# Kernel tuning notes

Measured on AMD Instinct MI355X. Metric: run time of the kernel, lower is better.

The kernel has to match this reference:

```python
import jax, jax.numpy as jnp
import numpy as np

N_CORES = 64
N_QUBITS = 1024
QEMB = 256
N_EDGES = 448
BATCH = 512
NN_DIMS = (256, 512, 512, 256)


def setup_inputs() -> dict:
    key = jax.random.key(0)
    ks = jax.random.split(key, 12)
    inp = {
        "core_allocs": jax.random.randint(ks[0], (BATCH, N_QUBITS), 0, N_CORES, dtype=jnp.int32),
        "qubit_embs": jax.random.normal(ks[1], (N_QUBITS, QEMB), dtype=jnp.float32),
        "dummy_qubit_emb": jax.random.normal(ks[2], (QEMB,), dtype=jnp.float32),
        "edge_index": jax.random.randint(ks[3], (2, N_EDGES), 0, N_CORES, dtype=jnp.int32),
        "edge_weight": jax.random.uniform(ks[4], (N_EDGES,), dtype=jnp.float32),
        "W1": jax.random.normal(ks[5], (NN_DIMS[0], NN_DIMS[1]), dtype=jnp.float32) * 0.05,
        "b1": jax.random.normal(ks[6], (NN_DIMS[1],), dtype=jnp.float32) * 0.05,
        "W2": jax.random.normal(ks[7], (NN_DIMS[1], NN_DIMS[2]), dtype=jnp.float32) * 0.05,
        "b2": jax.random.normal(ks[8], (NN_DIMS[2],), dtype=jnp.float32) * 0.05,
        "W3": jax.random.normal(ks[9], (NN_DIMS[2], NN_DIMS[3]), dtype=jnp.float32) * 0.05,
        "b3": jax.random.normal(ks[10], (NN_DIMS[3],), dtype=jnp.float32) * 0.05,
    }
    return inp


def _gcn_norm(edge_index, edge_weight):
    # PyG gcn_norm: add self loops (weight 1), symmetric D^{-1/2} A D^{-1/2}.
    self_idx = jnp.arange(N_CORES, dtype=edge_index.dtype)
    row = jnp.concatenate([edge_index[0], self_idx])
    col = jnp.concatenate([edge_index[1], self_idx])
    w = jnp.concatenate([edge_weight, jnp.ones((N_CORES,), edge_weight.dtype)])
    deg = jax.ops.segment_sum(w, col, num_segments=N_CORES)  # degree at targets
    dinv = jnp.where(deg > 0, deg ** -0.5, 0.0)
    norm = dinv[row] * w * dinv[col]
    return row, col, norm


def reference(core_allocs, qubit_embs, dummy_qubit_emb, edge_index, edge_weight,
              W1, b1, W2, b2, W3, b3):
    # ---- unmixedCoreEmbs, vectorized: per-core max over assigned qubit embs,
    # dummy emb always included (cores never at capacity) ----
    def pool(alloc):  # alloc: [n_qubits] -> [n_cores, qemb]
        seg = jax.ops.segment_max(qubit_embs, alloc, num_segments=N_CORES)
        return jnp.maximum(seg, dummy_qubit_emb)  # also fixes -inf empty cores

    x = jax.vmap(pool)(core_allocs)  # [B, n_cores, qemb]

    # ---- GCNConv stack (same graph replicated per batch element) ----
    row, col, norm = _gcn_norm(edge_index, edge_weight)

    def gcn_layer(h, W, b):
        hw = h @ W  # [B, C, d_out]
        msg = hw[:, row, :] * norm[None, :, None]  # gather sources, scale
        agg = jnp.zeros((h.shape[0], N_CORES, W.shape[1]), hw.dtype).at[:, col, :].add(msg)
        return jax.nn.relu(agg + b)

    x = gcn_layer(x, W1, b1)
    x = gcn_layer(x, W2, b2)
    x = gcn_layer(x, W3, b3)
    return x  # [B, n_cores, nn_dims[-1]] (original returns this split per batch element)
```

## Files before the change

kernel.cpp:

```cpp
#include <hip/hip_runtime.h>
#include <type_traits>

typedef __attribute__((ext_vector_type(8))) short short8;
typedef __attribute__((ext_vector_type(4))) short short4v;
typedef __attribute__((ext_vector_type(2))) short short2v;
typedef __attribute__((ext_vector_type(4))) float f32x4;
typedef unsigned short u16;
typedef unsigned int u32;

#define N_EDGES 448

#define WS_ADJA 0
#define WS_ADJB 4096
#define WS_W1   8192
#define WS_W2   139264
#define WS_W3   401408
#define WS_DUM  532480
#define WS_B1   (WS_DUM + 256)
#define WS_B2   (WS_DUM + 768)
#define WS_B3   (WS_DUM + 1280)
#define WS_QE   534528
#define WS_FLAG 796672

__device__ __forceinline__ float bf2f(u16 v) {
    u32 u = ((u32)v) << 16;
    return __builtin_bit_cast(float, u);
}
__device__ __forceinline__ u16 f2bf(float f) {
    u32 u = __builtin_bit_cast(u32, f);
    u32 r = u + 0x7FFFu + ((u >> 16) & 1u);
    return (u16)(r >> 16);
}
__device__ __forceinline__ u16 f2bf_fast(float f) {
    u32 u = __builtin_bit_cast(u32, f);
    return (u16)((u + 0x8000u) >> 16);
}
__device__ __forceinline__ float ldf(const void* p, int idx, u32 isf32) {
    return isf32 ? ((const float*)p)[idx] : bf2f(((const u16*)p)[idx]);
}
__device__ __forceinline__ u16 keyb(u16 b) {
    return (u16)(b ^ ((u16)(((u16)((short)b >> 15)) >> 1)));
}
__device__ __forceinline__ u32 pkmax(u32 a, u32 b) {
    short2v x = __builtin_bit_cast(short2v, a);
    short2v y = __builtin_bit_cast(short2v, b);
    short2v r = __builtin_elementwise_max(x, y);
    return __builtin_bit_cast(u32, r);
}

__global__ __launch_bounds__(512) void prep(
    const int* __restrict__ eidx, const void* __restrict__ ew,
    const void* __restrict__ qembs, const void* __restrict__ dummy,
    const void* __restrict__ W1, const void* __restrict__ b1,
    const void* __restrict__ W2, const void* __restrict__ b2,
    const void* __restrict__ W3, const void* __restrict__ b3,
    u16* __restrict__ ws) {
    const int t = threadIdx.x, bb = blockIdx.x;
    __shared__ u32 s_isf;
    if (t < 64) {
        const u16* qs = (const u16*)qembs;
        int c = 0;
#pragma unroll
        for (int j = 0; j < 4; j++) {
            u16 v = qs[(t * 4 + j) * 2];
            u32 e = (v >> 7) & 0xFF;
            c += (e >= 100 && e <= 134) ? 1 : 0;
        }
#pragma unroll
        for (int off = 32; off > 0; off >>= 1) c += __shfl_down(c, off, 64);
        if (t == 0) s_isf = (c < 128) ? 1u : 0u;
    }
    __syncthreads();
    const u32 isf32 = s_isf;

    if (t < 128) {
        const int bw = bb * 2 + (t >> 6);
        const int tl = t & 63;
        const void* src;
        int N, K32, dst, nt, kk;
        if (bw < 256)      { src = W1; N = 512; K32 = 8;  dst = WS_W1; nt = bw / 8;          kk = bw % 8; }
        else if (bw < 768) { src = W2; N = 512; K32 = 16; dst = WS_W2; nt = (bw - 256) / 16; kk = (bw - 256) % 16; }
        else               { src = W3; N = 256; K32 = 16; dst = WS_W3; nt = (bw - 768) / 16; kk = (bw - 768) % 16; }
        const int col = nt * 16 + (tl & 15);
        const int krow = kk * 32 + (tl >> 4) * 8;
        u16 v[8];
#pragma unroll
        for (int j = 0; j < 8; j++) v[j] = f2bf(ldf(src, (krow + j) * N + col, isf32));
        u16* o = ws + dst + (nt * K32 + kk) * 512 + tl * 8;
#pragma unroll
        for (int j = 0; j < 8; j++) o[j] = v[j];
    }
    if (t >= 256) {
        const int base = bb * 512 + (t - 256) * 2;
        ws[WS_QE + base]     = keyb(f2bf(ldf(qembs, base, isf32)));
        ws[WS_QE + base + 1] = keyb(f2bf(ldf(qembs, base + 1, isf32)));
    }
    if (bb == 1) {
#pragma unroll
        for (int j = 0; j < 4; j++) {
            int i = t + j * 512;
            if (i < 1792) {
                u16 o;
                if (i < 256)       o = keyb(f2bf(ldf(dummy, i, isf32)));
                else if (i < 768)  o = f2bf(ldf(b1, i - 256, isf32));
                else if (i < 1280) o = f2bf(ldf(b2, i - 768, isf32));
                else               o = f2bf(ldf(b3, i - 1280, isf32));
                ws[WS_DUM + i] = o;
            }
        }
    }
    if (bb == 0) {
        __shared__ float A[4096];
        __shared__ float deg[64];
        __shared__ float dinv[64];
        __shared__ int er[N_EDGES];
        __shared__ int ec[N_EDGES];
        __shared__ float ewf[N_EDGES];
        if (t < N_EDGES) {
            er[t] = eidx[t];
            ec[t] = eidx[N_EDGES + t];
            ewf[t] = ldf(ew, t, isf32);
        }
        if (t < 64) deg[t] = 1.0f;
        for (int i = t; i < 4096; i += 512) A[i] = 0.f;
        __syncthreads();
        if (t < N_EDGES) atomicAdd(&deg[ec[t]], ewf[t]);
        __syncthreads();
        if (t < 64) dinv[t] = 1.0f / sqrtf(deg[t]);
        __syncthreads();
        if (t < N_EDGES) atomicAdd(&A[ec[t] * 64 + er[t]], dinv[er[t]] * ewf[t] * dinv[ec[t]]);
        __syncthreads();
        if (t < 64) A[t * 64 + t] += dinv[t] * dinv[t];
        __syncthreads();
        for (int i = t; i < 4096; i += 512) {
            int chunk = i >> 9, m = (i >> 3) & 63, j = i & 7;
            ws[WS_ADJA + i] = f2bf(A[m * 64 + chunk * 8 + j]);
        }
        for (int i = t; i < 4096; i += 512) {
            int chunk = i >> 9, l = (i >> 3) & 63, j = i & 7;
            int ntc = chunk >> 1, kk = chunk & 1;
            int k = kk * 32 + (l >> 4) * 8 + j;
            int c2 = ntc * 16 + (l & 15);
            ws[WS_ADJB + i] = f2bf(A[c2 * 64 + k]);
        }
        if (t == 0) *(u32*)(ws + WS_FLAG) = isf32;
    }
}

__global__ __launch_bounds__(1024, 4) void fused(
    const int* __restrict__ allocs, const u16* __restrict__ ws,
    void* __restrict__ out) {

    __shared__ __align__(16) u16 BUF[64 * 512];

    const int t = threadIdx.x, bb = blockIdx.x;
    const int wave = t >> 6, lane = t & 63, quad = lane >> 4, nl = lane & 15;
    const u32 isf32 = *(const u32*)(ws + WS_FLAG);

    {
        int* LIST = (int*)(BUF + 16384);
        int* CNT  = LIST + 1024;
        int* SST  = CNT + 64;
        int* WOF  = SST + 64;
        if (t < 64) CNT[t] = 0;
        __syncthreads();
        const int myc = allocs[bb * 1024 + t];
        atomicAdd(&CNT[myc], 1);
        __syncthreads();
        if (t < 64) {
            int v = CNT[t], s = v;
#pragma unroll
            for (int off = 1; off < 64; off <<= 1) {
                int u = __shfl_up(s, off, 64);
                if (t >= off) s += u;
            }
            SST[t] = s - v;
            WOF[t] = s - v;
        }
        __syncthreads();
        {
            int pos = atomicAdd(&WOF[myc], 1);
            LIST[pos] = t;
        }
        __syncthreads();
        const u16* wsq = ws + WS_QE;
        const uint2 dk = *(const uint2*)(ws + WS_DUM + lane * 4);
        for (int i = 0; i < 4; i++) {
            const int c = wave * 4 + i;
            const int L = CNT[c], S = SST[c];
            u32 m0 = dk.x, m1 = dk.y;
            int j = 0;
            for (; j + 4 <= L; j += 4) {
                const int q0 = LIST[S + j],     q1 = LIST[S + j + 1];
                const int q2 = LIST[S + j + 2], q3 = LIST[S + j + 3];
                uint2 ra = *(const uint2*)(wsq + q0 * 256 + lane * 4);
                uint2 rb = *(const uint2*)(wsq + q1 * 256 + lane * 4);
                uint2 rc = *(const uint2*)(wsq + q2 * 256 + lane * 4);
                uint2 rd = *(const uint2*)(wsq + q3 * 256 + lane * 4);
                m0 = pkmax(pkmax(m0, ra.x), pkmax(rb.x, rc.x));
                m1 = pkmax(pkmax(m1, ra.y), pkmax(rb.y, rc.y));
                m0 = pkmax(m0, rd.x);
                m1 = pkmax(m1, rd.y);
            }
            for (; j < L; j++) {
                const int q = LIST[S + j];
                uint2 r = *(const uint2*)(wsq + q * 256 + lane * 4);
                m0 = pkmax(m0, r.x);
                m1 = pkmax(m1, r.y);
            }
            short4v p;
            p[0] = (short)keyb((u16)(m0 & 0xffffu));
            p[1] = (short)keyb((u16)(m0 >> 16));
            p[2] = (short)keyb((u16)(m1 & 0xffffu));
            p[3] = (short)keyb((u16)(m1 >> 16));
            *(short4v*)(BUF + (lane >> 1) * 512 + c * 8 + (lane & 1) * 4) = p;
        }
    }
    __syncthreads();

    short8 adjB[4][2];
#pragma unroll
    for (int ntc = 0; ntc < 4; ntc++)
#pragma unroll
        for (int h = 0; h < 2; h++)
            adjB[ntc][h] = *(const short8*)(ws + WS_ADJB + (ntc * 2 + h) * 512 + lane * 8);

    auto layerT = [&](auto K32c, const u16* __restrict__ W, const u16* __restrict__ bias) {
        constexpr int K32 = decltype(K32c)::value;
        const int s0 = wave * 2;
        u16* scr = BUF + (wave * 4 + 2) * 512;
        f32x4 acc[2][4];
#pragma unroll
        for (int s = 0; s < 2; s++)
#pragma unroll
            for (int rt = 0; rt < 4; rt++) acc[s][rt] = f32x4{0.f, 0.f, 0.f, 0.f};
#pragma unroll
        for (int kk = 0; kk < K32; kk++) {
            short8 a[4], bch[2];
#pragma unroll
            for (int rt = 0; rt < 4; rt++)
                a[rt] = *(const short8*)(BUF + (kk * 4 + quad) * 512 + (rt * 16 + nl) * 8);
#pragma unroll
            for (int s = 0; s < 2; s++)
                bch[s] = *(const short8*)(W + ((s0 + s) * K32 + kk) * 512 + lane * 8);
#pragma unroll
            for (int s = 0; s < 2; s++)
#pragma unroll
                for (int rt = 0; rt < 4; rt++)
                    acc[s][rt] = __builtin_amdgcn_mfma_f32_16x16x32_bf16(a[rt], bch[s], acc[s][rt], 0, 0, 0);
        }
        __syncthreads();
#pragma unroll
        for (int s = 0; s < 2; s++) {
            const int nt = s0 + s;
            f32x4 agg[4];
#pragma unroll
            for (int ntc = 0; ntc < 4; ntc++) agg[ntc] = f32x4{0.f, 0.f, 0.f, 0.f};
#pragma unroll
            for (int h = 0; h < 2; h++) {
#pragma unroll
                for (int r2 = 0; r2 < 2; r2++) {
                    f32x4 v = acc[s][2 * h + r2];
                    short4v p;
#pragma unroll
                    for (int rr = 0; rr < 4; rr++) p[rr] = (short)f2bf_fast(v[rr]);
                    *(short4v*)(scr + nl * 40 + r2 * 16 + quad * 4) = p;
                }
                short8 hwf = *(const short8*)(scr + nl * 40 + quad * 8);
#pragma unroll
                for (int ntc = 0; ntc < 4; ntc++)
                    agg[ntc] = __builtin_amdgcn_mfma_f32_16x16x32_bf16(hwf, adjB[ntc][h], agg[ntc], 0, 0, 0);
            }
            float bv[4];
#pragma unroll
            for (int rr = 0; rr < 4; rr++) bv[rr] = bf2f(bias[nt * 16 + quad * 4 + rr]);
#pragma unroll
            for (int ntc = 0; ntc < 4; ntc++) {
                short4v p;
#pragma unroll
                for (int rr = 0; rr < 4; rr++)
                    p[rr] = (short)f2bf_fast(fmaxf(agg[ntc][rr] + bv[rr], 0.f));
                *(short4v*)(BUF + (nt * 2 + (quad >> 1)) * 512 + (ntc * 16 + nl) * 8 + (quad & 1) * 4) = p;
            }
        }
        __syncthreads();
    };

    auto layer3 = [&](const u16* __restrict__ W) {
        const int nt = wave;
        f32x4 acc[4];
#pragma unroll
        for (int rt = 0; rt < 4; rt++) acc[rt] = f32x4{0.f, 0.f, 0.f, 0.f};
#pragma unroll
        for (int kk = 0; kk < 16; kk++) {
            short8 a[4];
#pragma unroll
            for (int rt = 0; rt < 4; rt++)
                a[rt] = *(const short8*)(BUF + (kk * 4 + quad) * 512 + (rt * 16 + nl) * 8);
            short8 bch = *(const short8*)(W + (nt * 16 + kk) * 512 + lane * 8);
#pragma unroll
            for (int rt = 0; rt < 4; rt++)
                acc[rt] = __builtin_amdgcn_mfma_f32_16x16x32_bf16(a[rt], bch, acc[rt], 0, 0, 0);
        }
        __syncthreads();
        u16* scr = BUF + 16384 + wave * 640;
#pragma unroll
        for (int h = 0; h < 2; h++) {
#pragma unroll
            for (int r2 = 0; r2 < 2; r2++) {
                f32x4 v = acc[2 * h + r2];
                short4v p;
#pragma unroll
                for (int rr = 0; rr < 4; rr++) p[rr] = (short)f2bf_fast(v[rr]);
                *(short4v*)(scr + nl * 40 + r2 * 16 + quad * 4) = p;
            }
            short8 hwf = *(const short8*)(scr + nl * 40 + quad * 8);
            *(short8*)(BUF + (nt * 2 + h) * 512 + lane * 8) = hwf;
        }
        __syncthreads();
    };

    layerT(std::integral_constant<int, 8>{},  ws + WS_W1, ws + WS_B1);
    layerT(std::integral_constant<int, 16>{}, ws + WS_W2, ws + WS_B2);
    layer3(ws + WS_W3);

    {
        const int rt2 = wave & 3, nt0 = (wave >> 2) * 4;
        short8 aA[2];
#pragma unroll
        for (int h = 0; h < 2; h++)
            aA[h] = *(const short8*)(ws + WS_ADJA + (h * 4 + quad) * 512 + (rt2 * 16 + nl) * 8);
        f32x4 accv[4];
#pragma unroll
        for (int ni = 0; ni < 4; ni++) {
            const int nt = nt0 + ni;
            short8 b0v = *(const short8*)(BUF + (nt * 2 + 0) * 512 + lane * 8);
            short8 b1v = *(const short8*)(BUF + (nt * 2 + 1) * 512 + lane * 8);
            f32x4 a = f32x4{0.f, 0.f, 0.f, 0.f};
            a = __builtin_amdgcn_mfma_f32_16x16x32_bf16(aA[0], b0v, a, 0, 0, 0);
            a = __builtin_amdgcn_mfma_f32_16x16x32_bf16(aA[1], b1v, a, 0, 0, 0);
            accv[ni] = a;
        }
        __syncthreads();
        float* Hf = (float*)BUF;
#pragma unroll
        for (int ni = 0; ni < 4; ni++) {
            const int n = (nt0 + ni) * 16 + nl;
            const float bv = bf2f(ws[WS_B3 + n]);
#pragma unroll
            for (int rr = 0; rr < 4; rr++) {
                const int m2 = rt2 * 16 + quad * 4 + rr;
                Hf[m2 * 256 + n] = fmaxf(accv[ni][rr] + bv, 0.f);
            }
        }
        __syncthreads();
        if (isf32) {
            float4* outv = (float4*)((float*)out + (size_t)bb * 16384);
            const float4* Hv = (const float4*)Hf;
#pragma unroll
            for (int p4 = 0; p4 < 4; p4++) outv[p4 * 1024 + t] = Hv[p4 * 1024 + t];
        } else {
            u16* outu = (u16*)out + (size_t)bb * 16384;
#pragma unroll
            for (int p4 = 0; p4 < 4; p4++) {
                const int idx = (p4 * 1024 + t) * 4;
                float4 v = *(const float4*)(Hf + idx);
                short4v pk;
                pk[0] = (short)f2bf_fast(v.x); pk[1] = (short)f2bf_fast(v.y);
                pk[2] = (short)f2bf_fast(v.z); pk[3] = (short)f2bf_fast(v.w);
                *(short4v*)(outu + idx) = pk;
            }
        }
    }
}

extern "C" void kernel_launch(void* const* d_in, const int* in_sizes, int n_in,
                              void* d_out, int out_size, void* d_ws, size_t ws_size,
                              hipStream_t stream) {
    const int* allocs = (const int*)d_in[0];
    const void* qembs = d_in[1];
    const void* dummy = d_in[2];
    const int* eidx   = (const int*)d_in[3];
    const void* ew    = d_in[4];
    const void* W1 = d_in[5];
    const void* b1 = d_in[6];
    const void* W2 = d_in[7];
    const void* b2 = d_in[8];
    const void* W3 = d_in[9];
    const void* b3 = d_in[10];
    u16* ws = (u16*)d_ws;

    prep<<<512, 512, 0, stream>>>(eidx, ew, qembs, dummy, W1, b1, W2, b2, W3, b3, ws);
    fused<<<512, 1024, 0, stream>>>(allocs, ws, d_out);
}
```

Baseline: 148.8 us.

## Process two batch elements per block to reuse weight fragments

Each block now handles two batch elements with double LDS buffers, so every weight fragment loaded from global memory feeds the MFMAs of both elements. The grid shrinks from 512 to 256 blocks. The adjacency B fragments move from registers into a shared-memory copy to save registers. The cost is double the LDS per block (about 136KB), which likely allows only one block per CU and leaves 256 blocks for a 256-CU device, so latency hiding and occupancy may suffer.

```diff
diff --git a/kernel.cpp b/kernel.cpp
--- a/kernel.cpp
+++ b/kernel.cpp
@@ -151,171 +151,204 @@
     const int* __restrict__ allocs, const u16* __restrict__ ws,
     void* __restrict__ out) {
 
-    __shared__ __align__(16) u16 BUF[64 * 512];
+    __shared__ __align__(16) u16 BUF[2][64 * 512];
+    __shared__ __align__(16) u16 ADJB_S[4096];
 
     const int t = threadIdx.x, bb = blockIdx.x;
     const int wave = t >> 6, lane = t & 63, quad = lane >> 4, nl = lane & 15;
     const u32 isf32 = *(const u32*)(ws + WS_FLAG);
+    const int e0 = bb * 2;
+
+    if (t < 512) *(uint4*)(ADJB_S + t * 8) = *(const uint4*)(ws + WS_ADJB + t * 8);
 
     {
-        int* LIST = (int*)(BUF + 16384);
-        int* CNT  = LIST + 1024;
-        int* SST  = CNT + 64;
-        int* WOF  = SST + 64;
-        if (t < 64) CNT[t] = 0;
-        __syncthreads();
-        const int myc = allocs[bb * 1024 + t];
-        atomicAdd(&CNT[myc], 1);
-        __syncthreads();
-        if (t < 64) {
-            int v = CNT[t], s = v;
+        int* LISTA = (int*)(BUF[0] + 16384);
+        int* CNTA  = LISTA + 1024;
+        int* SSTA  = CNTA + 64;
+        int* WOFA  = SSTA + 64;
+        int* LISTB = (int*)(BUF[1] + 16384);
+        int* CNTB  = LISTB + 1024;
+        int* SSTB  = CNTB + 64;
+        int* WOFB  = SSTB + 64;
+        if (t < 64) { CNTA[t] = 0; CNTB[t] = 0; }
+        __syncthreads();
+        const int ca = allocs[e0 * 1024 + t];
+        const int cb = allocs[(e0 + 1) * 1024 + t];
+        atomicAdd(&CNTA[ca], 1);
+        atomicAdd(&CNTB[cb], 1);
+        __syncthreads();
+        if (t < 128) {
+            const int l = t & 63;
+            int* C  = (t < 64) ? CNTA : CNTB;
+            int* S  = (t < 64) ? SSTA : SSTB;
+            int* Wo = (t < 64) ? WOFA : WOFB;
+            int v = C[l], s = v;
 #pragma unroll
             for (int off = 1; off < 64; off <<= 1) {
                 int u = __shfl_up(s, off, 64);
-                if (t >= off) s += u;
-            }
-            SST[t] = s - v;
-            WOF[t] = s - v;
+                if (l >= off) s += u;
+            }
+            S[l] = s - v;
+            Wo[l] = s - v;
         }
         __syncthreads();
         {
-            int pos = atomicAdd(&WOF[myc], 1);
-            LIST[pos] = t;
+            int pa = atomicAdd(&WOFA[ca], 1); LISTA[pa] = t;
+            int pb = atomicAdd(&WOFB[cb], 1); LISTB[pb] = t;
         }
         __syncthreads();
         const u16* wsq = ws + WS_QE;
         const uint2 dk = *(const uint2*)(ws + WS_DUM + lane * 4);
-        for (int i = 0; i < 4; i++) {
-            const int c = wave * 4 + i;
-            const int L = CNT[c], S = SST[c];
-            u32 m0 = dk.x, m1 = dk.y;
-            int j = 0;
-            for (; j + 4 <= L; j += 4) {
-                const int q0 = LIST[S + j],     q1 = LIST[S + j + 1];
-                const int q2 = LIST[S + j + 2], q3 = LIST[S + j + 3];
-                uint2 ra = *(const uint2*)(wsq + q0 * 256 + lane * 4);
-                uint2 rb = *(const uint2*)(wsq + q1 * 256 + lane * 4);
-                uint2 rc = *(const uint2*)(wsq + q2 * 256 + lane * 4);
-                uint2 rd = *(const uint2*)(wsq + q3 * 256 + lane * 4);
-                m0 = pkmax(pkmax(m0, ra.x), pkmax(rb.x, rc.x));
-                m1 = pkmax(pkmax(m1, ra.y), pkmax(rb.y, rc.y));
-                m0 = pkmax(m0, rd.x);
-                m1 = pkmax(m1, rd.y);
-            }
-            for (; j < L; j++) {
-                const int q = LIST[S + j];
-                uint2 r = *(const uint2*)(wsq + q * 256 + lane * 4);
-                m0 = pkmax(m0, r.x);
-                m1 = pkmax(m1, r.y);
-            }
-            short4v p;
-            p[0] = (short)keyb((u16)(m0 & 0xffffu));
-            p[1] = (short)keyb((u16)(m0 >> 16));
-            p[2] = (short)keyb((u16)(m1 & 0xffffu));
-            p[3] = (short)keyb((u16)(m1 >> 16));
-            *(short4v*)(BUF + (lane >> 1) * 512 + c * 8 + (lane & 1) * 4) = p;
+#pragma unroll
+        for (int e = 0; e < 2; e++) {
+            const int* LIST = e ? LISTB : LISTA;
+            const int* CNT  = e ? CNTB  : CNTA;
+            const int* SST  = e ? SSTB  : SSTA;
+            u16* XB = BUF[e];
+            for (int i = 0; i < 4; i++) {
+                const int c = wave * 4 + i;
+                const int L = CNT[c], S = SST[c];
+                u32 m0 = dk.x, m1 = dk.y;
+                int j = 0;
+                for (; j + 4 <= L; j += 4) {
+                    const int q0 = LIST[S + j],     q1 = LIST[S + j + 1];
+                    const int q2 = LIST[S + j + 2], q3 = LIST[S + j + 3];
+                    uint2 ra = *(const uint2*)(wsq + q0 * 256 + lane * 4);
+                    uint2 rb = *(const uint2*)(wsq + q1 * 256 + lane * 4);
+                    uint2 rc = *(const uint2*)(wsq + q2 * 256 + lane * 4);
+                    uint2 rd = *(const uint2*)(wsq + q3 * 256 + lane * 4);
+                    m0 = pkmax(pkmax(m0, ra.x), pkmax(rb.x, rc.x));
+                    m1 = pkmax(pkmax(m1, ra.y), pkmax(rb.y, rc.y));
+                    m0 = pkmax(m0, rd.x);
+                    m1 = pkmax(m1, rd.y);
+                }
+                for (; j < L; j++) {
+                    const int q = LIST[S + j];
+                    uint2 r = *(const uint2*)(wsq + q * 256 + lane * 4);
+                    m0 = pkmax(m0, r.x);
+                    m1 = pkmax(m1, r.y);
+                }
+                short4v p;
+                p[0] = (short)keyb((u16)(m0 & 0xffffu));
+                p[1] = (short)keyb((u16)(m0 >> 16));
+                p[2] = (short)keyb((u16)(m1 & 0xffffu));
+                p[3] = (short)keyb((u16)(m1 >> 16));
+                *(short4v*)(XB + (lane >> 1) * 512 + c * 8 + (lane & 1) * 4) = p;
+            }
         }
     }
     __syncthreads();
-
-    short8 adjB[4][2];
-#pragma unroll
-    for (int ntc = 0; ntc < 4; ntc++)
-#pragma unroll
-        for (int h = 0; h < 2; h++)
-            adjB[ntc][h] = *(const short8*)(ws + WS_ADJB + (ntc * 2 + h) * 512 + lane * 8);
 
     auto layerT = [&](auto K32c, const u16* __restrict__ W, const u16* __restrict__ bias) {
         constexpr int K32 = decltype(K32c)::value;
         const int s0 = wave * 2;
-        u16* scr = BUF + (wave * 4 + 2) * 512;
-        f32x4 acc[2][4];
-#pragma unroll
-        for (int s = 0; s < 2; s++)
-#pragma unroll
-            for (int rt = 0; rt < 4; rt++) acc[s][rt] = f32x4{0.f, 0.f, 0.f, 0.f};
+        f32x4 acc[2][2][4];
+#pragma unroll
+        for (int e = 0; e < 2; e++)
+#pragma unroll
+            for (int s = 0; s < 2; s++)
+#pragma unroll
+                for (int rt = 0; rt < 4; rt++) acc[e][s][rt] = f32x4{0.f, 0.f, 0.f, 0.f};
 #pragma unroll
         for (int kk = 0; kk < K32; kk++) {
-            short8 a[4], bch[2];
-#pragma unroll
-            for (int rt = 0; rt < 4; rt++)
-                a[rt] = *(const short8*)(BUF + (kk * 4 + quad) * 512 + (rt * 16 + nl) * 8);
+            short8 bch[2];
 #pragma unroll
             for (int s = 0; s < 2; s++)
                 bch[s] = *(const short8*)(W + ((s0 + s) * K32 + kk) * 512 + lane * 8);
 #pragma unroll
-            for (int s = 0; s < 2; s++)
+            for (int e = 0; e < 2; e++) {
+                short8 a[4];
 #pragma unroll
                 for (int rt = 0; rt < 4; rt++)
-                    acc[s][rt] = __builtin_amdgcn_mfma_f32_16x16x32_bf16(a[rt], bch[s], acc[s][rt], 0, 0, 0);
+                    a[rt] = *(const short8*)(BUF[e] + (kk * 4 + quad) * 512 + (rt * 16 + nl) * 8);
+#pragma unroll
+                for (int s = 0; s < 2; s++)
+#pragma unroll
+                    for (int rt = 0; rt < 4; rt++)
+                        acc[e][s][rt] = __builtin_amdgcn_mfma_f32_16x16x32_bf16(a[rt], bch[s], acc[e][s][rt], 0, 0, 0);
+            }
         }
         __syncthreads();
 #pragma unroll
         for (int s = 0; s < 2; s++) {
             const int nt = s0 + s;
-            f32x4 agg[4];
-#pragma unroll
-            for (int ntc = 0; ntc < 4; ntc++) agg[ntc] = f32x4{0.f, 0.f, 0.f, 0.f};
+            float bv[4];
+#pragma unroll
+            for (int rr = 0; rr < 4; rr++) bv[rr] = bf2f(bias[nt * 16 + quad * 4 + rr]);
+#pragma unroll
+            for (int e = 0; e < 2; e++) {
+                u16* scr = BUF[e] + (wave * 4 + 2) * 512;
+                f32x4 agg[4];
+#pragma unroll
+                for (int ntc = 0; ntc < 4; ntc++) agg[ntc] = f32x4{0.f, 0.f, 0.f, 0.f};
+#pragma unroll
+                for (int h = 0; h < 2; h++) {
+#pragma unroll
+                    for (int r2 = 0; r2 < 2; r2++) {
+                        f32x4 v = acc[e][s][2 * h + r2];
+                        short4v p;
+#pragma unroll
+                        for (int rr = 0; rr < 4; rr++) p[rr] = (short)f2bf_fast(v[rr]);
+                        *(short4v*)(scr + nl * 40 + r2 * 16 + quad * 4) = p;
+                    }
+                    short8 hwf = *(const short8*)(scr + nl * 40 + quad * 8);
+#pragma unroll
+                    for (int ntc = 0; ntc < 4; ntc++) {
+                        short8 bfrag = *(const short8*)(ADJB_S + (ntc * 2 + h) * 512 + lane * 8);
+                        agg[ntc] = __builtin_amdgcn_mfma_f32_16x16x32_bf16(hwf, bfrag, agg[ntc], 0, 0, 0);
+                    }
+                }
+#pragma unroll
+                for (int ntc = 0; ntc < 4; ntc++) {
+                    short4v p;
+#pragma unroll
+                    for (int rr = 0; rr < 4; rr++)
+                        p[rr] = (short)f2bf_fast(fmaxf(agg[ntc][rr] + bv[rr], 0.f));
+                    *(short4v*)(BUF[e] + (nt * 2 + (quad >> 1)) * 512 + (ntc * 16 + nl) * 8 + (quad & 1) * 4) = p;
+                }
+            }
+        }
+        __syncthreads();
+    };
+
+    auto layer3 = [&](const u16* __restrict__ W) {
+        const int nt = wave;
+        f32x4 acc[2][4];
+#pragma unroll
+        for (int e = 0; e < 2; e++)
+#pragma unroll
+            for (int rt = 0; rt < 4; rt++) acc[e][rt] = f32x4{0.f, 0.f, 0.f, 0.f};
+#pragma unroll
+        for (int kk = 0; kk < 16; kk++) {
+            short8 bch = *(const short8*)(W + (nt * 16 + kk) * 512 + lane * 8);
+#pragma unroll
+            for (int e = 0; e < 2; e++) {
+                short8 a[4];
+#pragma unroll
+                for (int rt = 0; rt < 4; rt++)
+                    a[rt] = *(const short8*)(BUF[e] + (kk * 4 + quad) * 512 + (rt * 16 + nl) * 8);
+#pragma unroll
+                for (int rt = 0; rt < 4; rt++)
+                    acc[e][rt] = __builtin_amdgcn_mfma_f32_16x16x32_bf16(a[rt], bch, acc[e][rt], 0, 0, 0);
+            }
+        }
+        __syncthreads();
+#pragma unroll
+        for (int e = 0; e < 2; e++) {
+            u16* scr = BUF[e] + 16384 + wave * 640;
 #pragma unroll
             for (int h = 0; h < 2; h++) {
 #pragma unroll
                 for (int r2 = 0; r2 < 2; r2++) {
-                    f32x4 v = acc[s][2 * h + r2];
+                    f32x4 v = acc[e][2 * h + r2];
                     short4v p;
 #pragma unroll
                     for (int rr = 0; rr < 4; rr++) p[rr] = (short)f2bf_fast(v[rr]);
                     *(short4v*)(scr + nl * 40 + r2 * 16 + quad * 4) = p;
                 }
                 short8 hwf = *(const short8*)(scr + nl * 40 + quad * 8);
-#pragma unroll
-                for (int ntc = 0; ntc < 4; ntc++)
-                    agg[ntc] = __builtin_amdgcn_mfma_f32_16x16x32_bf16(hwf, adjB[ntc][h], agg[ntc], 0, 0, 0);
-            }
-            float bv[4];
-#pragma unroll
-            for (int rr = 0; rr < 4; rr++) bv[rr] = bf2f(bias[nt * 16 + quad * 4 + rr]);
-#pragma unroll
-            for (int ntc = 0; ntc < 4; ntc++) {
-                short4v p;
-#pragma unroll
-                for (int rr = 0; rr < 4; rr++)
-                    p[rr] = (short)f2bf_fast(fmaxf(agg[ntc][rr] + bv[rr], 0.f));
-                *(short4v*)(BUF + (nt * 2 + (quad >> 1)) * 512 + (ntc * 16 + nl) * 8 + (quad & 1) * 4) = p;
-            }
-        }
-        __syncthreads();
-    };
-
-    auto layer3 = [&](const u16* __restrict__ W) {
-        const int nt = wave;
-        f32x4 acc[4];
-#pragma unroll
-        for (int rt = 0; rt < 4; rt++) acc[rt] = f32x4{0.f, 0.f, 0.f, 0.f};
-#pragma unroll
-        for (int kk = 0; kk < 16; kk++) {
-            short8 a[4];
-#pragma unroll
-            for (int rt = 0; rt < 4; rt++)
-                a[rt] = *(const short8*)(BUF + (kk * 4 + quad) * 512 + (rt * 16 + nl) * 8);
-            short8 bch = *(const short8*)(W + (nt * 16 + kk) * 512 + lane * 8);
-#pragma unroll
-            for (int rt = 0; rt < 4; rt++)
-                acc[rt] = __builtin_amdgcn_mfma_f32_16x16x32_bf16(a[rt], bch, acc[rt], 0, 0, 0);
-        }
-        __syncthreads();
-        u16* scr = BUF + 16384 + wave * 640;
-#pragma unroll
-        for (int h = 0; h < 2; h++) {
-#pragma unroll
-            for (int r2 = 0; r2 < 2; r2++) {
-                f32x4 v = acc[2 * h + r2];
-                short4v p;
-#pragma unroll
-                for (int rr = 0; rr < 4; rr++) p[rr] = (short)f2bf_fast(v[rr]);
-                *(short4v*)(scr + nl * 40 + r2 * 16 + quad * 4) = p;
-            }
-            short8 hwf = *(const short8*)(scr + nl * 40 + quad * 8);
-            *(short8*)(BUF + (nt * 2 + h) * 512 + lane * 8) = hwf;
+                *(short8*)(BUF[e] + (nt * 2 + h) * 512 + lane * 8) = hwf;
+            }
         }
         __syncthreads();
     };
@@ -330,45 +363,57 @@
 #pragma unroll
         for (int h = 0; h < 2; h++)
             aA[h] = *(const short8*)(ws + WS_ADJA + (h * 4 + quad) * 512 + (rt2 * 16 + nl) * 8);
-        f32x4 accv[4];
-#pragma unroll
-        for (int ni = 0; ni < 4; ni++) {
-            const int nt = nt0 + ni;
-            short8 b0v = *(const short8*)(BUF + (nt * 2 + 0) * 512 + lane * 8);
-            short8 b1v = *(const short8*)(BUF + (nt * 2 + 1) * 512 + lane * 8);
-            f32x4 a = f32x4{0.f, 0.f, 0.f, 0.f};
-            a = __builtin_amdgcn_mfma_f32_16x16x32_bf16(aA[0], b0v, a, 0, 0, 0);
-            a = __builtin_amdgcn_mfma_f32_16x16x32_bf16(aA[1], b1v, a, 0, 0, 0);
-            accv[ni] = a;
-        }
-        __syncthreads();
-        float* Hf = (float*)BUF;
-#pragma unroll
-        for (int ni = 0; ni < 4; ni++) {
-            const int n = (nt0 + ni) * 16 + nl;
-            const float bv = bf2f(ws[WS_B3 + n]);
-#pragma unroll
-            for (int rr = 0; rr < 4; rr++) {
-                const int m2 = rt2 * 16 + quad * 4 + rr;
-                Hf[m2 * 256 + n] = fmaxf(accv[ni][rr] + bv, 0.f);
+        f32x4 accv[2][4];
+#pragma unroll
+        for (int e = 0; e < 2; e++)
+#pragma unroll
+            for (int ni = 0; ni < 4; ni++) {
+                const int nt = nt0 + ni;
+                short8 b0v = *(const short8*)(BUF[e] + (nt * 2 + 0) * 512 + lane * 8);
+                short8 b1v = *(const short8*)(BUF[e] + (nt * 2 + 1) * 512 + lane * 8);
+                f32x4 a = f32x4{0.f, 0.f, 0.f, 0.f};
+                a = __builtin_amdgcn_mfma_f32_16x16x32_bf16(aA[0], b0v, a, 0, 0, 0);
+                a = __builtin_amdgcn_mfma_f32_16x16x32_bf16(aA[1], b1v, a, 0, 0, 0);
+                accv[e][ni] = a;
+            }
+        __syncthreads();
+#pragma unroll
+        for (int e = 0; e < 2; e++) {
+            float* Hf = (float*)BUF[e];
+#pragma unroll
+            for (int ni = 0; ni < 4; ni++) {
+                const int n = (nt0 + ni) * 16 + nl;
+                const float bv = bf2f(ws[WS_B3 + n]);
+#pragma unroll
+                for (int rr = 0; rr < 4; rr++) {
+                    const int m2 = rt2 * 16 + quad * 4 + rr;
+                    Hf[m2 * 256 + n] = fmaxf(accv[e][ni][rr] + bv, 0.f);
+                }
             }
         }
         __syncthreads();
         if (isf32) {
-            float4* outv = (float4*)((float*)out + (size_t)bb * 16384);
-            const float4* Hv = (const float4*)Hf;
-#pragma unroll
-            for (int p4 = 0; p4 < 4; p4++) outv[p4 * 1024 + t] = Hv[p4 * 1024 + t];
+#pragma unroll
+            for (int e = 0; e < 2; e++) {
+                float4* outv = (float4*)((float*)out + (size_t)(e0 + e) * 16384);
+                const float4* Hv = (const float4*)(BUF[e]);
+#pragma unroll
+                for (int p4 = 0; p4 < 4; p4++) outv[p4 * 1024 + t] = Hv[p4 * 1024 + t];
+            }
         } else {
-            u16* outu = (u16*)out + (size_t)bb * 16384;
-#pragma unroll
-            for (int p4 = 0; p4 < 4; p4++) {
-                const int idx = (p4 * 1024 + t) * 4;
-                float4 v = *(const float4*)(Hf + idx);
-                short4v pk;
-                pk[0] = (short)f2bf_fast(v.x); pk[1] = (short)f2bf_fast(v.y);
-                pk[2] = (short)f2bf_fast(v.z); pk[3] = (short)f2bf_fast(v.w);
-                *(short4v*)(outu + idx) = pk;
+#pragma unroll
+            for (int e = 0; e < 2; e++) {
+                u16* outu = (u16*)out + (size_t)(e0 + e) * 16384;
+                const float* Hf = (const float*)BUF[e];
+#pragma unroll
+                for (int p4 = 0; p4 < 4; p4++) {
+                    const int idx = (p4 * 1024 + t) * 4;
+                    float4 v = *(const float4*)(Hf + idx);
+                    short4v pk;
+                    pk[0] = (short)f2bf_fast(v.x); pk[1] = (short)f2bf_fast(v.y);
+                    pk[2] = (short)f2bf_fast(v.z); pk[3] = (short)f2bf_fast(v.w);
+                    *(short4v*)(outu + idx) = pk;
+                }
             }
         }
     }
@@ -391,5 +436,5 @@
     u16* ws = (u16*)d_ws;
 
     prep<<<512, 512, 0, stream>>>(eidx, ew, qembs, dummy, W1, b1, W2, b2, W3, b3, ws);
-    fused<<<512, 1024, 0, stream>>>(allocs, ws, d_out);
-}
+    fused<<<256, 1024, 0, stream>>>(allocs, ws, d_out);
+}
```

After: 141.2 us. 5.1% less time.
